# Kernel optimization log

Hardware: AMD Instinct MI355X
Metric: run time of the kernel (lower is better)

## Reference

```python
import jax, jax.numpy as jnp
import numpy as np

N, S, D = 2, 2048, 512
HEADS, HEAD_DIM = 8, 64
SCALE_BASE = 512.0
EPS = 1e-08


def xpos_apply(x, positions, downscale):
    # x: (B, S, d)  positions: (B, S) float
    d = x.shape[-1]
    half = jnp.arange(0, d, 2, dtype=jnp.float32)
    scale_vec = (half + 0.4 * d) / (1.4 * d)                      # (d/2,)
    power = positions[..., None] / SCALE_BASE                     # (B, S, 1)
    scale = scale_vec ** power                                    # (B, S, d/2)
    inv_freq = 1.0 / (10000.0 ** (half / d))                      # (d/2,)
    sinusoid = positions[..., None] * inv_freq                    # (B, S, d/2)
    sin = jnp.sin(sinusoid)
    cos = jnp.cos(sinusoid)
    if downscale:
        scale = 1.0 / scale
    # duplicate-interleave to full dim
    sin = jnp.repeat(sin, 2, axis=-1)
    cos = jnp.repeat(cos, 2, axis=-1)
    scale = jnp.repeat(scale, 2, axis=-1)
    x1 = x[..., 0::2]
    x2 = x[..., 1::2]
    rot = jnp.stack([-x2, x1], axis=-1).reshape(x.shape)          # rotate_every_two
    return (x * cos + rot * sin) * scale


def split_heads(x):
    # (N, S, H*Hd) -> (N*H, S, Hd)
    return x.reshape(N, S, HEADS, HEAD_DIM).transpose(0, 2, 1, 3).reshape(N * HEADS, S, HEAD_DIM)


def setup_inputs() -> dict:
    key = jax.random.key(0)
    ks = jax.random.split(key, 8)
    g = 1.0 / np.sqrt(D)
    return {
        'sequence': jax.random.normal(ks[0], (N, S, D), dtype=jnp.float32),
        'input_mask': jnp.ones((N, S), dtype=jnp.float32),
        'positions': jnp.tile(jnp.arange(S, dtype=jnp.int32), (N, 1)),
        'layer_num': 0,
        'Wq': jax.random.normal(ks[1], (D, D), dtype=jnp.float32) * g,
        'bq': jnp.zeros((D,), dtype=jnp.float32),
        'Wk': jax.random.normal(ks[2], (D, D), dtype=jnp.float32) * g,
        'bk': jnp.zeros((D,), dtype=jnp.float32),
        'Wv': jax.random.normal(ks[3], (D, D), dtype=jnp.float32) * g,
        'bv': jnp.zeros((D,), dtype=jnp.float32),
        'Wo': jax.random.normal(ks[4], (D, D), dtype=jnp.float32) * g,
        'bo': jnp.zeros((D,), dtype=jnp.float32),
    }


def reference(sequence, input_mask, positions, layer_num, Wq, bq, Wk, bk, Wv, bv, Wo, bo):
    scaling = HEAD_DIM ** (-0.5)
    posf = positions.astype(jnp.float32)

    Q = split_heads(sequence @ Wq.T + bq) * scaling               # (N*H, S, Hd)
    K = split_heads(sequence @ Wk.T + bk)
    V = split_heads(sequence @ Wv.T + bv)

    pos_h = jnp.repeat(posf, HEADS, axis=0)                       # 'n s -> (n h) s'
    K = xpos_apply(K, pos_h, downscale=True)
    Q = xpos_apply(Q, pos_h, downscale=False)

    A = jnp.einsum('nsd,ntd->nst', Q, K).reshape(N, HEADS, S, S)  # (N, H, S, S2)
    Vh = V.reshape(N, HEADS, S, HEAD_DIM)

    # causal mask: input_mask over kv dim, lower-triangular
    tri = jnp.tril(jnp.ones((S, S), dtype=jnp.float32))
    attn_mask = input_mask[:, None, None, :] * tri[None, None]    # (N, 1, S, S2)

    A = jax.nn.sigmoid(A) * attn_mask

    # stick-breaking decay: reverse-cumprod of (1 - A) along kv dim, shifted
    Af = jnp.flip(A, axis=(2, 3))
    C = jnp.exp(jnp.cumsum(jnp.log(1.0 - Af + EPS), axis=-1))
    C = jnp.flip(C, axis=(2, 3))
    C = jnp.concatenate([jnp.ones((N, HEADS, S, 1), dtype=C.dtype), C[..., :-1]], axis=-1)

    A = C * A
    attended = jnp.einsum('nhst,nhtd->nhsd', A, Vh)               # (N, H, S, Hd)
    attended = attended.transpose(0, 2, 1, 3).reshape(N, S, HEADS * HEAD_DIM)
    out = attended @ Wo.T + bo
    return out
```

## Files before the change

kernel.cpp:

```cpp
#include <hip/hip_runtime.h>
#include <math.h>

#define S_LEN 2048
#define DMODEL 512
#define HDIM 64
#define EPS_G 1e-8f

typedef __bf16 bf16x8 __attribute__((ext_vector_type(8)));
typedef __bf16 bf16x4 __attribute__((ext_vector_type(4)));
typedef float f32x4 __attribute__((ext_vector_type(4)));

template <int CTRL>
__device__ __forceinline__ float dpp_mov(float src, float oldv) {
  return __int_as_float(__builtin_amdgcn_update_dpp(
      __float_as_int(oldv), __float_as_int(src), CTRL, 0xF, 0xF, false));
}
#define ROW_SHL(n) (0x100 + (n))
#define ROW_SHR(n) (0x110 + (n))

__device__ __forceinline__ float swz_head(float v) {
  return __int_as_float(__builtin_amdgcn_ds_swizzle(__float_as_int(v), 0x0010));
}
__device__ __forceinline__ float swz_tail(float v) {
  return __int_as_float(__builtin_amdgcn_ds_swizzle(__float_as_int(v), 0x01F0));
}

__global__ __launch_bounds__(256) void cvt_kernel(
    const float* __restrict__ X, const float* __restrict__ Wq,
    const float* __restrict__ Wk, const float* __restrict__ Wv,
    const float* __restrict__ Wo,
    __bf16* __restrict__ Xb, __bf16* __restrict__ Wb, __bf16* __restrict__ Wob) {
  const int u = blockIdx.x * 256 + threadIdx.x;
  const float* src; __bf16* dst; int off;
  if (u < 524288)      { src = X;  dst = Xb;          off = u; }
  else if (u < 589824) { src = Wq; dst = Wb;          off = u - 524288; }
  else if (u < 655360) { src = Wk; dst = Wb + 262144; off = u - 589824; }
  else if (u < 720896) { src = Wv; dst = Wb + 524288; off = u - 655360; }
  else                 { src = Wo; dst = Wob;         off = u - 720896; }
  const float4 v = *(const float4*)(src + (size_t)off * 4);
  bf16x4 o;
  o[0] = (__bf16)v.x; o[1] = (__bf16)v.y; o[2] = (__bf16)v.z; o[3] = (__bf16)v.w;
  *(bf16x4*)(dst + (size_t)off * 4) = o;
}

__global__ __launch_bounds__(256, 2) void qkv_gemm(
    const __bf16* __restrict__ Xb, const __bf16* __restrict__ Wb,
    const float* __restrict__ bq, const float* __restrict__ bk, const float* __restrict__ bv,
    const int* __restrict__ pos,
    __bf16* __restrict__ Qh, __bf16* __restrict__ Kh, __bf16* __restrict__ Vt) {
  const int i0 = blockIdx.x << 6;
  const int h  = blockIdx.y;
  const int j0 = h << 6;

  __shared__ __bf16 Xs[64][72];
  __shared__ __bf16 Wls[3][64][72];

  const int tid = threadIdx.x;
  const int wv = tid >> 6, lane = tid & 63;
  const int l = lane & 15, seg = lane >> 4;
  const int sr = tid >> 2, sc = (tid & 3) << 4;

  f32x4 O[3][4];
#pragma unroll
  for (int w = 0; w < 3; ++w)
#pragma unroll
    for (int r4 = 0; r4 < 4; ++r4) O[w][r4] = (f32x4){0.f, 0.f, 0.f, 0.f};

  bf16x8 xr0, xr1, wr[3][2];
#define LOADQKV(K0)                                                                   \
  {                                                                                   \
    const __bf16* xp = Xb + (size_t)(i0 + sr) * 512 + (K0) + sc;                      \
    xr0 = *(const bf16x8*)xp; xr1 = *(const bf16x8*)(xp + 8);                         \
    _Pragma("unroll")                                                                 \
    for (int w = 0; w < 3; ++w) {                                                     \
      const __bf16* wp = Wb + (size_t)w * 262144 + (size_t)(j0 + sr) * 512 + (K0) + sc;\
      wr[w][0] = *(const bf16x8*)wp; wr[w][1] = *(const bf16x8*)(wp + 8);             \
    }                                                                                 \
  }

  LOADQKV(0)
  for (int k0 = 0; k0 < 512; k0 += 64) {
    __syncthreads();
    *(bf16x8*)&Xs[sr][sc]     = xr0;
    *(bf16x8*)&Xs[sr][sc + 8] = xr1;
#pragma unroll
    for (int w = 0; w < 3; ++w) {
      *(bf16x8*)&Wls[w][sr][sc]     = wr[w][0];
      *(bf16x8*)&Wls[w][sr][sc + 8] = wr[w][1];
    }
    __syncthreads();
    if (k0 < 448) LOADQKV(k0 + 64)

    bf16x8 a0[4], a1[4];
#pragma unroll
    for (int r4 = 0; r4 < 4; ++r4) {
      a0[r4] = *(const bf16x8*)&Xs[r4 * 16 + l][seg * 8];
      a1[r4] = *(const bf16x8*)&Xs[r4 * 16 + l][seg * 8 + 32];
    }
#pragma unroll
    for (int w = 0; w < 3; ++w) {
      bf16x8 b0 = *(const bf16x8*)&Wls[w][wv * 16 + l][seg * 8];
      bf16x8 b1 = *(const bf16x8*)&Wls[w][wv * 16 + l][seg * 8 + 32];
#pragma unroll
      for (int r4 = 0; r4 < 4; ++r4) {
        O[w][r4] = __builtin_amdgcn_mfma_f32_16x16x32_bf16(a0[r4], b0, O[w][r4], 0, 0, 0);
        O[w][r4] = __builtin_amdgcn_mfma_f32_16x16x32_bf16(a1[r4], b1, O[w][r4], 0, 0, 0);
      }
    }
  }

  const int d = wv * 16 + l;
  const float bbq = bq[j0 + d], bbk = bk[j0 + d], bbv = bv[j0 + d];
#pragma unroll
  for (int r4 = 0; r4 < 4; ++r4)
#pragma unroll
    for (int reg = 0; reg < 4; ++reg) {
      O[0][r4][reg] += bbq; O[1][r4][reg] += bbk; O[2][r4][reg] += bbv;
    }

  const int n = i0 >> 11, sb = i0 & 2047;
  const int nh = (n << 3) + h;

  const float kp   = (float)(d >> 1);
  const float invf = exp2f(-0.41524100f * kp) * 0.15915494f;
  const float l2sv = log2f((2.f * kp + 25.6f) * (1.f / 89.6f));
  float pv_[4][4];
#pragma unroll
  for (int r4 = 0; r4 < 4; ++r4)
#pragma unroll
    for (int reg = 0; reg < 4; ++reg)
      pv_[r4][reg] = (float)pos[n * S_LEN + sb + r4 * 16 + (seg << 2) + reg];

  __syncthreads();

#pragma unroll
  for (int r4 = 0; r4 < 4; ++r4)
#pragma unroll
    for (int reg = 0; reg < 4; ++reg) {
      const int row = r4 * 16 + (seg << 2) + reg;
      const float p = pv_[r4][reg];
      const float rev0 = p * invf;
      const float rev  = rev0 - floorf(rev0);
      const float sn = __builtin_amdgcn_sinf(rev);
      const float cn = __builtin_amdgcn_cosf(rev);
      const float sq = exp2f(p * (1.f / 512.f) * l2sv);
      const float sQ = sq * 0.125f;
      const float sK = __builtin_amdgcn_rcpf(sq);
      float x  = O[0][r4][reg];
      float xp = __shfl_xor(x, 1);
      Xs[row][d] = (__bf16)((((d & 1) ? (x * cn + xp * sn) : (x * cn - xp * sn))) * sQ);
      x  = O[1][r4][reg];
      xp = __shfl_xor(x, 1);
      Wls[0][row][d] = (__bf16)((((d & 1) ? (x * cn + xp * sn) : (x * cn - xp * sn))) * sK);
      Wls[1][row][d] = (__bf16)O[2][r4][reg];
    }
  __syncthreads();

  __bf16* qdst = Qh + (((size_t)nh * S_LEN + sb + sr) << 6) + sc;
  *(bf16x8*)qdst       = *(bf16x8*)&Xs[sr][sc];
  *(bf16x8*)(qdst + 8) = *(bf16x8*)&Xs[sr][sc + 8];
  __bf16* kdst = Kh + (((size_t)nh * S_LEN + sb + sr) << 6) + sc;
  *(bf16x8*)kdst       = *(bf16x8*)&Wls[0][sr][sc];
  *(bf16x8*)(kdst + 8) = *(bf16x8*)&Wls[0][sr][sc + 8];

  const int dv = tid >> 2, part = tid & 3;
  __bf16 tmp[16];
#pragma unroll
  for (int i = 0; i < 16; ++i) tmp[i] = Wls[1][part * 16 + i][dv];
  __bf16* vdst = Vt + (((size_t)(nh * 64 + dv)) << 11) + sb + part * 16;
  *(bf16x8*)vdst       = *(bf16x8*)&tmp[0];
  *(bf16x8*)(vdst + 8) = *(bf16x8*)&tmp[8];
}

__global__ __launch_bounds__(256, 4) void attn_chunk(
    const __bf16* __restrict__ Qh, const __bf16* __restrict__ Kh,
    const __bf16* __restrict__ Vt, const float* __restrict__ imask,
    __bf16* __restrict__ att, float* __restrict__ PartO,
    float* __restrict__ PartP, float* __restrict__ PartA0) {
  const int id = 1279 - (int)blockIdx.x;
  const int nh = id & 15;
  const int t  = id >> 4;
  int rb, c, nc;
  if (t < 8)       { rb = t; c = 0; nc = 1; }
  else if (t < 24) { int u = t - 8;  rb = 8  + (u >> 1); c = u & 1;     nc = 2; }
  else if (t < 48) { int u = t - 24; rb = 16 + u / 3;    c = u - 3 * (u / 3); nc = 3; }
  else             { int u = t - 48; rb = 24 + (u >> 2); c = u & 3;     nc = 4; }
  const int T   = rb + 1;
  const int bsz = T / nc;
  const int rem = T - bsz * nc;
  const int szc  = bsz + ((c < rem) ? 1 : 0);
  const int skip = c * bsz + ((c < rem) ? c : rem);
  const int hi = rb - skip;
  const int lo = hi - szc + 1;

  const int n = nh >> 3, h = nh & 7;
  const int tid = threadIdx.x;
  const int wv = tid >> 6, lane = tid & 63;
  const int l = lane & 15, seg = lane >> 4;
  const int pr = tid >> 3, pc = (tid & 7) << 3;

  __shared__ __bf16 Ks16[64][72];
  __shared__ __bf16 Vt16[64][72];
  __shared__ __bf16 cs16[64][72];
  __shared__ float msk[64];

  const __bf16* qbase =
      Qh + (((size_t)nh * S_LEN + rb * 64 + wv * 16 + l) << 6);
  const bf16x8 aq0 = *(const bf16x8*)(qbase + seg * 8);
  const bf16x8 aq1 = *(const bf16x8*)(qbase + seg * 8 + 32);

  f32x4 O[4];
  float pend[4][4];
  float Crow[4];
  float a0k0[4];
#pragma unroll
  for (int nt = 0; nt < 4; ++nt) O[nt] = (f32x4){0.f, 0.f, 0.f, 0.f};
#pragma unroll
  for (int r = 0; r < 4; ++r) {
    Crow[r] = 1.f; a0k0[r] = 0.f;
#pragma unroll
    for (int nt = 0; nt < 4; ++nt) pend[r][nt] = 0.f;
  }

  bf16x8 kp0, kp1, vp0, vp1;
  float mp = 0.f;
#define LOADKV(JT)                                                                     \
  kp0 = *(const bf16x8*)(Kh + (((size_t)nh * S_LEN + (JT) * 64 + pr) << 6) + pc);      \
  kp1 = *(const bf16x8*)(Kh + (((size_t)nh * S_LEN + (JT) * 64 + 32 + pr) << 6) + pc); \
  vp0 = *(const bf16x8*)(Vt + (((size_t)(nh * 64 + pr)) << 11) + (JT) * 64 + pc);      \
  vp1 = *(const bf16x8*)(Vt + (((size_t)(nh * 64 + 32 + pr)) << 11) + (JT) * 64 + pc); \
  if (tid < 64) mp = imask[n * S_LEN + (JT) * 64 + tid];

  LOADKV(hi)

  for (int jt = hi; jt >= lo; --jt) {
    __syncthreads();
    *(bf16x8*)&Ks16[pr][pc]      = kp0;
    *(bf16x8*)&Ks16[32 + pr][pc] = kp1;
    *(bf16x8*)&Vt16[pr][pc]      = vp0;
    *(bf16x8*)&Vt16[32 + pr][pc] = vp1;
    if (tid < 64) msk[tid] = mp;
    __syncthreads();
    if (jt > lo) { LOADKV(jt - 1) }

    f32x4 Sv[4];
    __builtin_amdgcn_s_setprio(1);
#pragma unroll
    for (int nt = 0; nt < 4; ++nt) {
      bf16x8 bk0 = *(const bf16x8*)&Ks16[nt * 16 + l][seg * 8];
      bf16x8 bk1 = *(const bf16x8*)&Ks16[nt * 16 + l][seg * 8 + 32];
      f32x4 z = (f32x4){0.f, 0.f, 0.f, 0.f};
      z = __builtin_amdgcn_mfma_f32_16x16x32_bf16(aq0, bk0, z, 0, 0, 0);
      z = __builtin_amdgcn_mfma_f32_16x16x32_bf16(aq1, bk1, z, 0, 0, 0);
      Sv[nt] = z;
    }
    __builtin_amdgcn_s_setprio(0);

    float v0f[4];
#pragma unroll
    for (int nt = 0; nt < 4; ++nt) v0f[nt] = (float)Vt16[nt * 16 + l][0];

    float mv_[4];
#pragma unroll
    for (int nt = 0; nt < 4; ++nt) mv_[nt] = msk[nt * 16 + l];

    const bool diag  = (jt == rb);
    const int  kbase = jt * 64 + l;

#pragma unroll
    for (int reg = 0; reg < 4; ++reg) {
      const int qrow = rb * 64 + wv * 16 + seg * 4 + reg;
      float a_[4], f_[4], p_[4];
#pragma unroll
      for (int nt = 0; nt < 4; ++nt) {
        const float s = Sv[nt][reg];
        a_[nt] = mv_[nt] * __builtin_amdgcn_rcpf(1.f + __expf(-s));
      }
      if (diag) {
#pragma unroll
        for (int nt = 0; nt < 4; ++nt)
          if (kbase + nt * 16 > qrow) a_[nt] = 0.f;
      }
#pragma unroll
      for (int nt = 0; nt < 4; ++nt) f_[nt] = 1.f - a_[nt] + EPS_G;
#pragma unroll
      for (int nt = 0; nt < 4; ++nt) {
        float p = f_[nt];
        p *= dpp_mov<ROW_SHL(1)>(p, 1.f);
        p *= dpp_mov<ROW_SHL(2)>(p, 1.f);
        p *= dpp_mov<ROW_SHL(4)>(p, 1.f);
        p *= dpp_mov<ROW_SHL(8)>(p, 1.f);
        p_[nt] = p;
      }
      float P_[4], tl[4];
#pragma unroll
      for (int nt = 0; nt < 4; ++nt) {
        P_[nt] = swz_head(p_[nt]);
        tl[nt] = swz_tail(f_[nt]);
      }
      const float a0 = swz_head(a_[0]);
      const float crow = Crow[reg];
      const float T2 = P_[3], T1 = T2 * P_[2], T0 = T1 * P_[1];
      const float TC[4] = {T0 * crow, T1 * crow, T2 * crow, crow};
      const float Ptile = T0 * P_[0];
#pragma unroll
      for (int nt = 0; nt < 4; ++nt) {
        const float bnd = (nt == 0) ? 0.f : tl[nt - 1] * P_[nt];
        const float sel = dpp_mov<ROW_SHR(1)>(p_[nt], bnd);
        float cv = a_[nt] * sel * TC[nt];
        if (nt == 0 && jt == 0 && nc == 1 && l == 0) cv = a_[0];
        cs16[wv * 16 + seg * 4 + reg][nt * 16 + l] = (__bf16)cv;
      }
      if (jt == 0) a0k0[reg] = a0;
      const float f63 = tl[3];
      const float s0  = a0 * Ptile * crow;
      Crow[reg] = crow * Ptile;
#pragma unroll
      for (int nt = 0; nt < 4; ++nt) {
        O[nt][reg] += pend[reg][nt] * f63;
        pend[reg][nt] = s0 * v0f[nt];
      }
    }

    bf16x8 ac0 = *(const bf16x8*)&cs16[wv * 16 + l][seg * 8];
    bf16x8 ac1 = *(const bf16x8*)&cs16[wv * 16 + l][seg * 8 + 32];
    __builtin_amdgcn_s_setprio(1);
#pragma unroll
    for (int nt = 0; nt < 4; ++nt) {
      bf16x8 bv0 = *(const bf16x8*)&Vt16[nt * 16 + l][seg * 8];
      bf16x8 bv1 = *(const bf16x8*)&Vt16[nt * 16 + l][seg * 8 + 32];
      O[nt] = __builtin_amdgcn_mfma_f32_16x16x32_bf16(ac0, bv0, O[nt], 0, 0, 0);
      O[nt] = __builtin_amdgcn_mfma_f32_16x16x32_bf16(ac1, bv1, O[nt], 0, 0, 0);
    }
    __builtin_amdgcn_s_setprio(0);
  }

  if (lo > 0) {
    const int m = lo << 6;
    const float mb = imask[n * S_LEN + m - 1];
    const __bf16* kb = Kh + (((size_t)nh * S_LEN + m - 1) << 6) + seg * 16;
    bf16x8 kb0 = *(const bf16x8*)kb, kb1 = *(const bf16x8*)(kb + 8);
    bf16x8 q0 = *(const bf16x8*)(qbase + seg * 16);
    bf16x8 q1 = *(const bf16x8*)(qbase + seg * 16 + 8);
    float sc_ = 0.f;
#pragma unroll
    for (int j = 0; j < 8; ++j)
      sc_ += (float)q0[j] * (float)kb0[j] + (float)q1[j] * (float)kb1[j];
    sc_ += __shfl_xor(sc_, 16);
    sc_ += __shfl_xor(sc_, 32);
    const float fbl = 1.f - mb * __builtin_amdgcn_rcpf(1.f + __expf(-sc_)) + EPS_G;
#pragma unroll
    for (int reg = 0; reg < 4; ++reg) {
      const float fb = __shfl(fbl, (seg << 2) + reg);
#pragma unroll
      for (int nt = 0; nt < 4; ++nt) O[nt][reg] += pend[reg][nt] * fb;
    }
  }

  if (nc == 1) {
#pragma unroll
    for (int nt = 0; nt < 4; ++nt)
#pragma unroll
      for (int reg = 0; reg < 4; ++reg) {
        const int srow = rb * 64 + wv * 16 + seg * 4 + reg;
        att[((size_t)(n * S_LEN + srow)) * DMODEL + h * HDIM + nt * 16 + l] =
            (__bf16)O[nt][reg];
      }
  } else {
    const int slot = nh * 72 + (t - 8);
    float* po = PartO + (size_t)slot * 4096;
#pragma unroll
    for (int nt = 0; nt < 4; ++nt)
#pragma unroll
      for (int reg = 0; reg < 4; ++reg)
        po[(wv * 16 + seg * 4 + reg) * 64 + nt * 16 + l] = O[nt][reg];
    if (l == 0) {
#pragma unroll
      for (int reg = 0; reg < 4; ++reg)
        PartP[slot * 64 + wv * 16 + seg * 4 + reg] = Crow[reg];
      if (lo == 0) {
#pragma unroll
        for (int reg = 0; reg < 4; ++reg)
          PartA0[(nh * 24 + rb - 8) * 64 + wv * 16 + seg * 4 + reg] = a0k0[reg];
      }
    }
  }
}

__global__ __launch_bounds__(256) void combine_kernel(
    const float* __restrict__ PartO, const float* __restrict__ PartP,
    const float* __restrict__ PartA0, const __bf16* __restrict__ Vt,
    __bf16* __restrict__ att) {
  const int b = blockIdx.x;
  const int nh = b / 24;
  const int rb = 8 + (b - nh * 24);
  const int nc = (rb < 16) ? 2 : ((rb < 24) ? 3 : 4);
  const int t0 = (rb < 16) ? 8 + ((rb - 8) << 1)
               : (rb < 24) ? 24 + (rb - 16) * 3
                           : 48 + ((rb - 24) << 2);
  const int n = nh >> 3, h = nh & 7;
  const int tid = threadIdx.x;
  const int r = tid >> 2, db = (tid & 3) << 4;

  float acc[16];
#pragma unroll
  for (int j = 0; j < 16; ++j) acc[j] = 0.f;
  float fac = 1.f;
  for (int c = 0; c < nc; ++c) {
    const int slot = nh * 72 + (t0 - 8) + c;
    const float* po = PartO + (size_t)slot * 4096 + r * 64 + db;
    const float P = PartP[slot * 64 + r];
#pragma unroll
    for (int q = 0; q < 4; ++q) {
      const float4 v = *(const float4*)(po + q * 4);
      acc[q * 4 + 0] += fac * v.x; acc[q * 4 + 1] += fac * v.y;
      acc[q * 4 + 2] += fac * v.z; acc[q * 4 + 3] += fac * v.w;
    }
    fac *= P;
  }
  const float a0 = PartA0[(nh * 24 + rb - 8) * 64 + r];
#pragma unroll
  for (int j = 0; j < 16; ++j)
    acc[j] += a0 * (float)Vt[(((size_t)(nh * 64 + db + j)) << 11)];

  __bf16 ob[16];
#pragma unroll
  for (int j = 0; j < 16; ++j) ob[j] = (__bf16)acc[j];
  __bf16* dst = att + ((size_t)(n * S_LEN + rb * 64 + r)) * DMODEL + h * HDIM + db;
  *(bf16x8*)dst       = *(bf16x8*)&ob[0];
  *(bf16x8*)(dst + 8) = *(bf16x8*)&ob[8];
}

__global__ __launch_bounds__(256, 2) void out_gemm(const __bf16* __restrict__ Xa,
                                                   const __bf16* __restrict__ Wob,
                                                   const float* __restrict__ bo,
                                                   float* __restrict__ Out) {
  const int i0 = blockIdx.x << 6, j0 = blockIdx.y << 7;
  __shared__ __bf16 As[64][72];
  __shared__ __bf16 Bs[128][72];

  const int tid = threadIdx.x;
  const int wv = tid >> 6, lane = tid & 63;
  const int l = lane & 15, seg = lane >> 4;
  const int sr = tid >> 2, sc = (tid & 3) << 4;

  f32x4 O[2][4];
#pragma unroll
  for (int j = 0; j < 2; ++j)
#pragma unroll
    for (int r4 = 0; r4 < 4; ++r4) O[j][r4] = (f32x4){0.f, 0.f, 0.f, 0.f};

  bf16x8 ar0, ar1, br[2][2];
#define LOADOUT(K0)                                                          \
  {                                                                          \
    const __bf16* xp = Xa + (size_t)(i0 + sr) * 512 + (K0) + sc;             \
    ar0 = *(const bf16x8*)xp; ar1 = *(const bf16x8*)(xp + 8);                \
    _Pragma("unroll")                                                        \
    for (int ps = 0; ps < 2; ++ps) {                                         \
      const __bf16* wp = Wob + (size_t)(j0 + ps * 64 + sr) * 512 + (K0) + sc;\
      br[ps][0] = *(const bf16x8*)wp; br[ps][1] = *(const bf16x8*)(wp + 8);  \
    }                                                                        \
  }

  LOADOUT(0)
  for (int k0 = 0; k0 < 512; k0 += 64) {
    __syncthreads();
    *(bf16x8*)&As[sr][sc]     = ar0;
    *(bf16x8*)&As[sr][sc + 8] = ar1;
#pragma unroll
    for (int ps = 0; ps < 2; ++ps) {
      *(bf16x8*)&Bs[ps * 64 + sr][sc]     = br[ps][0];
      *(bf16x8*)&Bs[ps * 64 + sr][sc + 8] = br[ps][1];
    }
    __syncthreads();
    if (k0 < 448) LOADOUT(k0 + 64)

    bf16x8 a0[4], a1[4];
#pragma unroll
    for (int r4 = 0; r4 < 4; ++r4) {
      a0[r4] = *(const bf16x8*)&As[r4 * 16 + l][seg * 8];
      a1[r4] = *(const bf16x8*)&As[r4 * 16 + l][seg * 8 + 32];
    }
#pragma unroll
    for (int j = 0; j < 2; ++j) {
      const int u = wv + 4 * j;
      bf16x8 b0 = *(const bf16x8*)&Bs[u * 16 + l][seg * 8];
      bf16x8 b1 = *(const bf16x8*)&Bs[u * 16 + l][seg * 8 + 32];
#pragma unroll
      for (int r4 = 0; r4 < 4; ++r4) {
        O[j][r4] = __builtin_amdgcn_mfma_f32_16x16x32_bf16(a0[r4], b0, O[j][r4], 0, 0, 0);
        O[j][r4] = __builtin_amdgcn_mfma_f32_16x16x32_bf16(a1[r4], b1, O[j][r4], 0, 0, 0);
      }
    }
  }

#pragma unroll
  for (int j = 0; j < 2; ++j) {
    const int u = wv + 4 * j;
    const float bb = bo[j0 + u * 16 + l];
#pragma unroll
    for (int r4 = 0; r4 < 4; ++r4)
#pragma unroll
      for (int reg = 0; reg < 4; ++reg) {
        const int m = r4 * 16 + (seg << 2) + reg;
        Out[(size_t)(i0 + m) * 512 + j0 + u * 16 + l] = O[j][r4][reg] + bb;
      }
  }
}

extern "C" void kernel_launch(void* const* d_in, const int* in_sizes, int n_in,
                              void* d_out, int out_size, void* d_ws, size_t ws_size,
                              hipStream_t stream) {
  (void)in_sizes; (void)n_in; (void)out_size; (void)ws_size;
  const float* seq  = (const float*)d_in[0];
  const float* mask = (const float*)d_in[1];
  const int*   pos  = (const int*)d_in[2];
  const float* Wq = (const float*)d_in[4];
  const float* bq = (const float*)d_in[5];
  const float* Wk = (const float*)d_in[6];
  const float* bk = (const float*)d_in[7];
  const float* Wv = (const float*)d_in[8];
  const float* bv = (const float*)d_in[9];
  const float* Wo = (const float*)d_in[10];
  const float* bo = (const float*)d_in[11];
  float* out = (float*)d_out;

  char* base = (char*)d_ws;
  __bf16* att = (__bf16*)base;
  __bf16* Qh  = (__bf16*)(base + ( 4u << 20));
  __bf16* Kh  = (__bf16*)(base + ( 8u << 20));
  __bf16* Vt  = (__bf16*)(base + (12u << 20));
  __bf16* Wb  = (__bf16*)(base + (16u << 20));
  __bf16* Wob = (__bf16*)(base + (18u << 20));
  __bf16* Xb  = (__bf16*)(base + (19u << 20));
  float* PartO  = (float*)(base + (23u << 20));
  float* PartP  = (float*)(base + (42u << 20));
  float* PartA0 = (float*)(base + (43u << 20));

  cvt_kernel<<<3072, 256, 0, stream>>>(seq, Wq, Wk, Wv, Wo, Xb, Wb, Wob);
  qkv_gemm<<<dim3(64, 8), 256, 0, stream>>>(Xb, Wb, bq, bk, bv, pos, Qh, Kh, Vt);
  attn_chunk<<<1280, 256, 0, stream>>>(Qh, Kh, Vt, mask, att, PartO, PartP, PartA0);
  combine_kernel<<<384, 256, 0, stream>>>(PartO, PartP, PartA0, Vt, att);
  out_gemm<<<dim3(64, 4), 256, 0, stream>>>(att, Wob, bo, out);
}
```

Baseline: 163.1 us.

## Transpose MFMA operand layout so each lane owns a query row in attn_chunk

Measured after the change: 148.9 us. -8.7%, faster.

```diff
diff --git a/kernel.cpp b/kernel.cpp
--- a/kernel.cpp
+++ b/kernel.cpp
@@ -9,21 +9,6 @@
 typedef __bf16 bf16x8 __attribute__((ext_vector_type(8)));
 typedef __bf16 bf16x4 __attribute__((ext_vector_type(4)));
 typedef float f32x4 __attribute__((ext_vector_type(4)));
-
-template <int CTRL>
-__device__ __forceinline__ float dpp_mov(float src, float oldv) {
-  return __int_as_float(__builtin_amdgcn_update_dpp(
-      __float_as_int(oldv), __float_as_int(src), CTRL, 0xF, 0xF, false));
-}
-#define ROW_SHL(n) (0x100 + (n))
-#define ROW_SHR(n) (0x110 + (n))
-
-__device__ __forceinline__ float swz_head(float v) {
-  return __int_as_float(__builtin_amdgcn_ds_swizzle(__float_as_int(v), 0x0010));
-}
-__device__ __forceinline__ float swz_tail(float v) {
-  return __int_as_float(__builtin_amdgcn_ds_swizzle(__float_as_int(v), 0x01F0));
-}
 
 __global__ __launch_bounds__(256) void cvt_kernel(
     const float* __restrict__ X, const float* __restrict__ Wq,
@@ -172,7 +157,7 @@
   *(bf16x8*)(vdst + 8) = *(bf16x8*)&tmp[8];
 }
 
-__global__ __launch_bounds__(256, 4) void attn_chunk(
+__global__ __launch_bounds__(256, 2) void attn_chunk(
     const __bf16* __restrict__ Qh, const __bf16* __restrict__ Kh,
     const __bf16* __restrict__ Vt, const float* __restrict__ imask,
     __bf16* __restrict__ att, float* __restrict__ PartO,
@@ -197,12 +182,14 @@
   const int tid = threadIdx.x;
   const int wv = tid >> 6, lane = tid & 63;
   const int l = lane & 15, seg = lane >> 4;
+  const int sg4 = seg << 2;
   const int pr = tid >> 3, pc = (tid & 7) << 3;
 
   __shared__ __bf16 Ks16[64][72];
   __shared__ __bf16 Vt16[64][72];
   __shared__ __bf16 cs16[64][72];
   __shared__ float msk[64];
+  __shared__ float v0buf[64];
 
   const __bf16* qbase =
       Qh + (((size_t)nh * S_LEN + rb * 64 + wv * 16 + l) << 6);
@@ -210,16 +197,13 @@
   const bf16x8 aq1 = *(const bf16x8*)(qbase + seg * 8 + 32);
 
   f32x4 O[4];
-  float pend[4][4];
-  float Crow[4];
-  float a0k0[4];
-#pragma unroll
-  for (int nt = 0; nt < 4; ++nt) O[nt] = (f32x4){0.f, 0.f, 0.f, 0.f};
-#pragma unroll
-  for (int r = 0; r < 4; ++r) {
-    Crow[r] = 1.f; a0k0[r] = 0.f;
-#pragma unroll
-    for (int nt = 0; nt < 4; ++nt) pend[r][nt] = 0.f;
+  f32x4 pend[4];
+  float Crow = 1.f;
+  float a0k0 = 0.f;
+#pragma unroll
+  for (int d_ = 0; d_ < 4; ++d_) {
+    O[d_] = (f32x4){0.f, 0.f, 0.f, 0.f};
+    pend[d_] = (f32x4){0.f, 0.f, 0.f, 0.f};
   }
 
   bf16x8 kp0, kp1, vp0, vp1;
@@ -240,6 +224,10 @@
     *(bf16x8*)&Vt16[pr][pc]      = vp0;
     *(bf16x8*)&Vt16[32 + pr][pc] = vp1;
     if (tid < 64) msk[tid] = mp;
+    if ((tid & 7) == 0) {
+      v0buf[pr]      = (float)vp0[0];
+      v0buf[32 + pr] = (float)vp1[0];
+    }
     __syncthreads();
     if (jt > lo) { LOADKV(jt - 1) }
 
@@ -250,87 +238,107 @@
       bf16x8 bk0 = *(const bf16x8*)&Ks16[nt * 16 + l][seg * 8];
       bf16x8 bk1 = *(const bf16x8*)&Ks16[nt * 16 + l][seg * 8 + 32];
       f32x4 z = (f32x4){0.f, 0.f, 0.f, 0.f};
-      z = __builtin_amdgcn_mfma_f32_16x16x32_bf16(aq0, bk0, z, 0, 0, 0);
-      z = __builtin_amdgcn_mfma_f32_16x16x32_bf16(aq1, bk1, z, 0, 0, 0);
+      z = __builtin_amdgcn_mfma_f32_16x16x32_bf16(bk0, aq0, z, 0, 0, 0);
+      z = __builtin_amdgcn_mfma_f32_16x16x32_bf16(bk1, aq1, z, 0, 0, 0);
       Sv[nt] = z;
     }
     __builtin_amdgcn_s_setprio(0);
 
-    float v0f[4];
-#pragma unroll
-    for (int nt = 0; nt < 4; ++nt) v0f[nt] = (float)Vt16[nt * 16 + l][0];
-
-    float mv_[4];
-#pragma unroll
-    for (int nt = 0; nt < 4; ++nt) mv_[nt] = msk[nt * 16 + l];
-
-    const bool diag  = (jt == rb);
-    const int  kbase = jt * 64 + l;
-
-#pragma unroll
-    for (int reg = 0; reg < 4; ++reg) {
-      const int qrow = rb * 64 + wv * 16 + seg * 4 + reg;
-      float a_[4], f_[4], p_[4];
-#pragma unroll
-      for (int nt = 0; nt < 4; ++nt) {
-        const float s = Sv[nt][reg];
-        a_[nt] = mv_[nt] * __builtin_amdgcn_rcpf(1.f + __expf(-s));
-      }
-      if (diag) {
-#pragma unroll
-        for (int nt = 0; nt < 4; ++nt)
-          if (kbase + nt * 16 > qrow) a_[nt] = 0.f;
-      }
-#pragma unroll
-      for (int nt = 0; nt < 4; ++nt) f_[nt] = 1.f - a_[nt] + EPS_G;
-#pragma unroll
-      for (int nt = 0; nt < 4; ++nt) {
-        float p = f_[nt];
-        p *= dpp_mov<ROW_SHL(1)>(p, 1.f);
-        p *= dpp_mov<ROW_SHL(2)>(p, 1.f);
-        p *= dpp_mov<ROW_SHL(4)>(p, 1.f);
-        p *= dpp_mov<ROW_SHL(8)>(p, 1.f);
-        p_[nt] = p;
-      }
-      float P_[4], tl[4];
-#pragma unroll
-      for (int nt = 0; nt < 4; ++nt) {
-        P_[nt] = swz_head(p_[nt]);
-        tl[nt] = swz_tail(f_[nt]);
-      }
-      const float a0 = swz_head(a_[0]);
-      const float crow = Crow[reg];
-      const float T2 = P_[3], T1 = T2 * P_[2], T0 = T1 * P_[1];
-      const float TC[4] = {T0 * crow, T1 * crow, T2 * crow, crow};
-      const float Ptile = T0 * P_[0];
-#pragma unroll
-      for (int nt = 0; nt < 4; ++nt) {
-        const float bnd = (nt == 0) ? 0.f : tl[nt - 1] * P_[nt];
-        const float sel = dpp_mov<ROW_SHR(1)>(p_[nt], bnd);
-        float cv = a_[nt] * sel * TC[nt];
-        if (nt == 0 && jt == 0 && nc == 1 && l == 0) cv = a_[0];
-        cs16[wv * 16 + seg * 4 + reg][nt * 16 + l] = (__bf16)cv;
-      }
-      if (jt == 0) a0k0[reg] = a0;
-      const float f63 = tl[3];
-      const float s0  = a0 * Ptile * crow;
-      Crow[reg] = crow * Ptile;
-#pragma unroll
-      for (int nt = 0; nt < 4; ++nt) {
-        O[nt][reg] += pend[reg][nt] * f63;
-        pend[reg][nt] = s0 * v0f[nt];
-      }
-    }
-
-    bf16x8 ac0 = *(const bf16x8*)&cs16[wv * 16 + l][seg * 8];
-    bf16x8 ac1 = *(const bf16x8*)&cs16[wv * 16 + l][seg * 8 + 32];
+    const bool diag = (jt == rb);
+    const int qoff = wv * 16 + l;
+
+    float a_[4][4];
+#pragma unroll
+    for (int nt = 0; nt < 4; ++nt) {
+      const float4 m4 = *(const float4*)&msk[nt * 16 + sg4];
+      a_[nt][0] = m4.x * __builtin_amdgcn_rcpf(1.f + __expf(-Sv[nt][0]));
+      a_[nt][1] = m4.y * __builtin_amdgcn_rcpf(1.f + __expf(-Sv[nt][1]));
+      a_[nt][2] = m4.z * __builtin_amdgcn_rcpf(1.f + __expf(-Sv[nt][2]));
+      a_[nt][3] = m4.w * __builtin_amdgcn_rcpf(1.f + __expf(-Sv[nt][3]));
+    }
+    if (diag) {
+#pragma unroll
+      for (int nt = 0; nt < 4; ++nt)
+#pragma unroll
+        for (int reg = 0; reg < 4; ++reg)
+          if (nt * 16 + sg4 + reg > qoff) a_[nt][reg] = 0.f;
+    }
+
+    float t_[4][4], gp[4], f3s[4];
+#pragma unroll
+    for (int nt = 0; nt < 4; ++nt) {
+      const float f0 = 1.f - a_[nt][0] + EPS_G;
+      const float f1 = 1.f - a_[nt][1] + EPS_G;
+      const float f2 = 1.f - a_[nt][2] + EPS_G;
+      const float f3 = 1.f - a_[nt][3] + EPS_G;
+      t_[nt][3] = f3;
+      t_[nt][2] = f2 * f3;
+      t_[nt][1] = f1 * t_[nt][2];
+      t_[nt][0] = f0 * t_[nt][1];
+      gp[nt] = t_[nt][0];
+      f3s[nt] = f3;
+    }
+
+    float S_[4], GP[4], Xs_[4], Yb[4];
+#pragma unroll
+    for (int nt = 0; nt < 4; ++nt) {
+      const float b = __shfl_xor(gp[nt], 16);
+      const float cc = __shfl_xor(gp[nt], 32);
+      const float dd = __shfl_xor(b, 32);
+      const float cd = cc * dd;
+      const float low  = (seg & 1) ? cd : b * cd;
+      const float high = (seg & 1) ? 1.f : b;
+      S_[nt] = (seg & 2) ? high : low;
+      GP[nt] = gp[nt] * b * cd;
+      Xs_[nt] = __shfl_up(f3s[nt], 16);
+      Yb[nt] = __shfl(f3s[nt], 48 + l);
+    }
+    const float T2 = GP[3], T1 = T2 * GP[2], T0 = T1 * GP[1];
+    const float Tarr[4] = {T0, T1, T2, 1.f};
+    const float Ptile = T0 * GP[0];
+    const float A0 = __shfl(a_[0][0], l);
+
+#pragma unroll
+    for (int nt = 0; nt < 4; ++nt) {
+      const float wc = S_[nt] * Tarr[nt] * Crow;
+      float cv0 = a_[nt][0] * Xs_[nt] * gp[nt] * wc;
+      const float cv0s0 = (nt == 0)
+          ? ((jt == 0 && nc == 1) ? a_[0][0] : 0.f)
+          : a_[nt][0] * Yb[nt - 1] * Tarr[nt - 1] * Crow;
+      if (seg == 0) cv0 = cv0s0;
+      const float cv1 = a_[nt][1] * t_[nt][0] * wc;
+      const float cv2 = a_[nt][2] * t_[nt][1] * wc;
+      const float cv3 = a_[nt][3] * t_[nt][2] * wc;
+      bf16x4 pk;
+      pk[0] = (__bf16)cv0; pk[1] = (__bf16)cv1;
+      pk[2] = (__bf16)cv2; pk[3] = (__bf16)cv3;
+      *(bf16x4*)&cs16[wv * 16 + l][nt * 16 + sg4] = pk;
+    }
+
+    const float f63 = Yb[3];
+    const float s0 = A0 * Ptile * Crow;
+    Crow *= Ptile;
+    if (jt == 0) a0k0 = A0;
+#pragma unroll
+    for (int dblk = 0; dblk < 4; ++dblk) {
+      O[dblk][0] += pend[dblk][0] * f63;
+      O[dblk][1] += pend[dblk][1] * f63;
+      O[dblk][2] += pend[dblk][2] * f63;
+      O[dblk][3] += pend[dblk][3] * f63;
+      const float4 v4 = *(const float4*)&v0buf[dblk * 16 + sg4];
+      pend[dblk][0] = s0 * v4.x; pend[dblk][1] = s0 * v4.y;
+      pend[dblk][2] = s0 * v4.z; pend[dblk][3] = s0 * v4.w;
+    }
+
+    bf16x8 bc0 = *(const bf16x8*)&cs16[wv * 16 + l][seg * 8];
+    bf16x8 bc1 = *(const bf16x8*)&cs16[wv * 16 + l][seg * 8 + 32];
     __builtin_amdgcn_s_setprio(1);
 #pragma unroll
-    for (int nt = 0; nt < 4; ++nt) {
-      bf16x8 bv0 = *(const bf16x8*)&Vt16[nt * 16 + l][seg * 8];
-      bf16x8 bv1 = *(const bf16x8*)&Vt16[nt * 16 + l][seg * 8 + 32];
-      O[nt] = __builtin_amdgcn_mfma_f32_16x16x32_bf16(ac0, bv0, O[nt], 0, 0, 0);
-      O[nt] = __builtin_amdgcn_mfma_f32_16x16x32_bf16(ac1, bv1, O[nt], 0, 0, 0);
+    for (int dblk = 0; dblk < 4; ++dblk) {
+      bf16x8 av0 = *(const bf16x8*)&Vt16[dblk * 16 + l][seg * 8];
+      bf16x8 av1 = *(const bf16x8*)&Vt16[dblk * 16 + l][seg * 8 + 32];
+      O[dblk] = __builtin_amdgcn_mfma_f32_16x16x32_bf16(av0, bc0, O[dblk], 0, 0, 0);
+      O[dblk] = __builtin_amdgcn_mfma_f32_16x16x32_bf16(av1, bc1, O[dblk], 0, 0, 0);
     }
     __builtin_amdgcn_s_setprio(0);
   }
@@ -350,39 +358,36 @@
     sc_ += __shfl_xor(sc_, 32);
     const float fbl = 1.f - mb * __builtin_amdgcn_rcpf(1.f + __expf(-sc_)) + EPS_G;
 #pragma unroll
-    for (int reg = 0; reg < 4; ++reg) {
-      const float fb = __shfl(fbl, (seg << 2) + reg);
-#pragma unroll
-      for (int nt = 0; nt < 4; ++nt) O[nt][reg] += pend[reg][nt] * fb;
+    for (int dblk = 0; dblk < 4; ++dblk) {
+      O[dblk][0] += pend[dblk][0] * fbl;
+      O[dblk][1] += pend[dblk][1] * fbl;
+      O[dblk][2] += pend[dblk][2] * fbl;
+      O[dblk][3] += pend[dblk][3] * fbl;
     }
   }
 
   if (nc == 1) {
-#pragma unroll
-    for (int nt = 0; nt < 4; ++nt)
-#pragma unroll
-      for (int reg = 0; reg < 4; ++reg) {
-        const int srow = rb * 64 + wv * 16 + seg * 4 + reg;
-        att[((size_t)(n * S_LEN + srow)) * DMODEL + h * HDIM + nt * 16 + l] =
-            (__bf16)O[nt][reg];
-      }
+    __bf16* arow = att + ((size_t)(n * S_LEN + rb * 64 + wv * 16 + l)) * DMODEL + h * HDIM;
+#pragma unroll
+    for (int dblk = 0; dblk < 4; ++dblk) {
+      bf16x4 ob;
+      ob[0] = (__bf16)O[dblk][0]; ob[1] = (__bf16)O[dblk][1];
+      ob[2] = (__bf16)O[dblk][2]; ob[3] = (__bf16)O[dblk][3];
+      *(bf16x4*)(arow + dblk * 16 + sg4) = ob;
+    }
   } else {
     const int slot = nh * 72 + (t - 8);
-    float* po = PartO + (size_t)slot * 4096;
-#pragma unroll
-    for (int nt = 0; nt < 4; ++nt)
-#pragma unroll
-      for (int reg = 0; reg < 4; ++reg)
-        po[(wv * 16 + seg * 4 + reg) * 64 + nt * 16 + l] = O[nt][reg];
-    if (l == 0) {
-#pragma unroll
-      for (int reg = 0; reg < 4; ++reg)
-        PartP[slot * 64 + wv * 16 + seg * 4 + reg] = Crow[reg];
-      if (lo == 0) {
-#pragma unroll
-        for (int reg = 0; reg < 4; ++reg)
-          PartA0[(nh * 24 + rb - 8) * 64 + wv * 16 + seg * 4 + reg] = a0k0[reg];
-      }
+    float* po = PartO + (size_t)slot * 4096 + (wv * 16 + l) * 64;
+#pragma unroll
+    for (int dblk = 0; dblk < 4; ++dblk) {
+      float4 v;
+      v.x = O[dblk][0]; v.y = O[dblk][1]; v.z = O[dblk][2]; v.w = O[dblk][3];
+      *(float4*)(po + dblk * 16 + sg4) = v;
+    }
+    if (seg == 0) {
+      PartP[slot * 64 + wv * 16 + l] = Crow;
+      if (lo == 0)
+        PartA0[(nh * 24 + rb - 8) * 64 + wv * 16 + l] = a0k0;
     }
   }
 }
```
